# Performance work log

Hardware: AMD Instinct MI355X
Metric: run time of the kernel (lower is better)

## Reference

```python
import jax, jax.numpy as jnp
import numpy as np

B, S, E, O, LAYERS = 256, 28, 256, 256, 3


def setup_inputs() -> dict:
    key = jax.random.key(0)
    ks = jax.random.split(key, 20)
    sc = 0.05
    inp = {
        "centers": jax.random.normal(ks[0], (B, S, 3), jnp.float32),
        "object_embedding": jax.random.normal(ks[1], (B, S, E), jnp.float32),
        "counts": jax.random.randint(ks[2], (B,), 1, S + 1),
        # linear_relation_object: 3 -> E
        "Wr": jax.random.normal(ks[3], (E, 3), jnp.float32) * sc,
        "br": jnp.zeros((E,), jnp.float32),
        # LSTM (PyTorch gate order i,f,g,o)
        "W_ih": jax.random.normal(ks[4], (4 * O, E), jnp.float32) * sc,
        "W_hh": jax.random.normal(ks[5], (4 * O, O), jnp.float32) * sc,
        "b_ih": jnp.zeros((4 * O,), jnp.float32),
        "b_hh": jnp.zeros((4 * O,), jnp.float32),
        # gr: 3E -> O
        "Wgr": jax.random.normal(ks[6], (O, 3 * E), jnp.float32) * sc,
        "bgr": jnp.zeros((O,), jnp.float32),
        # bezier control: O -> O, plus scalar alpha
        "Wbc": jax.random.normal(ks[7], (O, O), jnp.float32) * sc,
        "bbc": jnp.zeros((O,), jnp.float32),
        "alpha": jnp.asarray(0.5, jnp.float32),
        # esa: E -> O
        "Wesa": jax.random.normal(ks[8], (O, E), jnp.float32) * sc,
        "besa": jnp.zeros((O,), jnp.float32),
        # gaussian heads: O -> 3
        "Wmu": jax.random.normal(ks[9], (3, O), jnp.float32) * sc,
        "bmu": jnp.zeros((3,), jnp.float32),
        "Wlv": jax.random.normal(ks[10], (3, O), jnp.float32) * sc,
        "blv": jnp.zeros((3,), jnp.float32),
    }
    return inp


def _lstm(x, W_ih, W_hh, b_ih, b_hh):
    # x: [B,S,E] -> hs: [B,S,O], zero initial state, PyTorch gate order i,f,g,o
    Bdim = x.shape[0]
    Odim = W_hh.shape[1]
    b = b_ih + b_hh

    def step(carry, xt):
        h, c = carry
        z = xt @ W_ih.T + h @ W_hh.T + b  # [B,4O]
        i, f, g, o = jnp.split(z, 4, axis=-1)
        c = jax.nn.sigmoid(f) * c + jax.nn.sigmoid(i) * jnp.tanh(g)
        h = jax.nn.sigmoid(o) * jnp.tanh(c)
        return (h, c), h

    h0 = jnp.zeros((Bdim, Odim), x.dtype)
    _, hs = jax.lax.scan(step, (h0, h0), jnp.swapaxes(x, 0, 1))
    return jnp.swapaxes(hs, 0, 1)


def reference(centers, object_embedding, counts, Wr, br, W_ih, W_hh, b_ih, b_hh,
              Wgr, bgr, Wbc, bbc, alpha, Wesa, besa, Wmu, bmu, Wlv, blv):
    # masks from per-scene object counts (padding replication of the torch loops)
    idx = jnp.arange(S)
    obj_mask = (idx[None, :] < counts[:, None]).astype(jnp.float32)[..., None]  # [B,S,1]
    rel_mask = (obj_mask[:, :, None, :] * obj_mask[:, None, :, :])              # [B,S,S,1]

    centers_p = centers * obj_mask                     # padded centers are zero
    relation = centers_p[:, :, None, :] - centers_p[:, None, :, :]  # [B,S,S,3]
    rlf = relation @ Wr.T + br                         # [B,S,S,E]

    olf = object_embedding * obj_mask                  # [B,S,E]
    t = jax.nn.sigmoid(alpha)

    for _ in range(LAYERS):
        new_olf = _lstm(olf, W_ih, W_hh, b_ih, b_hh) * obj_mask
        rep_i = jnp.broadcast_to(olf[:, :, None, :], (olf.shape[0], S, S, olf.shape[-1]))
        rep_j = jnp.broadcast_to(olf[:, None, :, :], (olf.shape[0], S, S, olf.shape[-1]))
        cat = jnp.concatenate([rep_i, rep_j, rlf], axis=-1)   # [B,S,S,3E]
        rlf_lin = cat @ Wgr.T + bgr                           # [B,S,S,O]
        cp = rlf_lin @ Wbc.T + bbc
        bez = ((1 - t) ** 2 + t ** 2) * rlf_lin + 2 * (1 - t) * t * cp
        rlf = jnp.tanh(bez) * rel_mask
        olf = new_olf

    rlf = rlf @ Wesa.T + besa                                  # [B,S,S,O]
    # base attention: softmax over dim=1 (explicit max-subtract as in source)
    base_attn = jax.nn.softmax(rlf - jnp.max(rlf, axis=1, keepdims=True), axis=1)
    # gaussian attention (eval mode: eps = 0 -> samples = mus)
    mus = rlf @ Wmu.T + bmu                                    # [B,S,S,3]
    _logvars = rlf @ Wlv.T + blv                               # computed, unused at eval
    gscores = jnp.mean(mus, axis=-1, keepdims=True)            # [B,S,S,1]
    gattn = jax.nn.softmax(gscores, axis=1)
    attn = 0.5 * base_attn + 0.5 * gattn                       # broadcast over O
    rel_out = jnp.sum(attn * rlf, axis=-2) * obj_mask          # [B,S,O]
    return rel_out
```

## Files before the change

kernel.cpp:

```cpp
#include <hip/hip_runtime.h>


typedef __attribute__((ext_vector_type(8))) short short8;
typedef __attribute__((ext_vector_type(4))) float f32x4;

__device__ __forceinline__ float b2f(unsigned short u){
  union { unsigned int i; float f; } v; v.i = ((unsigned int)u) << 16; return v.f;
}
__device__ __forceinline__ float u2f(unsigned int u){
  union { unsigned int i; float f; } v; v.i = u; return v.f;
}
__device__ __forceinline__ unsigned short f2b(float f){
  union { float f; unsigned int i; } v; v.f = f;
  return (unsigned short)((v.i + 0x8000u) >> 16);
}
__device__ __forceinline__ unsigned int pk2(float lo, float hi){
  union { float f; unsigned int i; } a, b; a.f = lo; b.f = hi;
  return __builtin_amdgcn_perm(b.i + 0x8000u, a.i + 0x8000u, 0x07060302u);
}
__device__ __forceinline__ float sigm(float x){ return 1.f/(1.f+__expf(-x)); }
__device__ __forceinline__ float tanh_f(float x){ float e = __expf(2.f*x); return 1.f - 2.f/(e+1.f); }
__device__ __forceinline__ int xsw(int row, int n){
  int c = n >> 3;
  int pc = (c & 24) | ((c ^ row) & 7);
  return row*256 + pc*8 + (n & 7);
}

#define MFMA16(a,b,c) __builtin_amdgcn_mfma_f32_16x16x32_bf16((a),(b),(c),0,0,0)

__global__ __launch_bounds__(256) void k_repack7(const float* __restrict__ Wih,
                                                 const float* __restrict__ Whh,
                                                 const float* __restrict__ Wgr,
                                                 const float* __restrict__ Wbc,
                                                 const float* __restrict__ Wesa,
                                                 const float* __restrict__ Wmu,
                                                 unsigned short* __restrict__ wcv,
                                                 float* __restrict__ wmean){
  int i = blockIdx.x*256 + threadIdx.x;
  if (i >= 851968){
    int o = i - 851968;
    if (o < 256) wmean[o] = (Wmu[o] + Wmu[256+o] + Wmu[512+o]) * (1.f/3.f);
    return;
  }
  const float* s; int segbase, N, stride, off, local;
  if      (i < 262144){ s=Wih;  segbase=0;      N=1024; stride=256; off=0;   local=i; }
  else if (i < 524288){ s=Whh;  segbase=262144; N=1024; stride=256; off=0;   local=i-262144; }
  else if (i < 589824){ s=Wgr;  segbase=524288; N=256;  stride=768; off=0;   local=i-524288; }
  else if (i < 655360){ s=Wgr;  segbase=589824; N=256;  stride=768; off=256; local=i-589824; }
  else if (i < 720896){ s=Wgr;  segbase=655360; N=256;  stride=768; off=512; local=i-655360; }
  else if (i < 786432){ s=Wbc;  segbase=720896; N=256;  stride=256; off=0;   local=i-720896; }
  else                { s=Wesa; segbase=786432; N=256;  stride=256; off=0;   local=i-786432; }
  int n = local >> 8, k = local & 255;
  wcv[segbase + (((k >> 3)*N + n) << 3) + (k & 7)] = f2b(s[n*stride + off + k]);
}

__global__ __launch_bounds__(256) void k_prep(const float* __restrict__ emb,
                                              const int* __restrict__ counts,
                                              unsigned short* __restrict__ olf,
                                              float* __restrict__ out){
  int bs = blockIdx.x;
  int b = bs / 28; int s = bs - b*28;
  int e = threadIdx.x;
  olf[(size_t)bs*256 + e] = (s < counts[b]) ? f2b(emb[(size_t)bs*256 + e]) : (unsigned short)0;
  out[(size_t)bs*256 + e] = 0.f;
}

__global__ __launch_bounds__(256) void k_xgemm(const unsigned short* __restrict__ olf,
                                               const unsigned short* __restrict__ Wih,
                                               unsigned short* __restrict__ zx){
  const int tid = threadIdx.x;
  const int wid = tid >> 6, lane = tid & 63, col = lane & 15, quad = lane >> 4;
  const int m0 = (blockIdx.x >> 1)*64 + wid*16;
  const int nt0 = (blockIdx.x & 1)*32;
  short8 af[8];
  #pragma unroll
  for (int kt=0; kt<8; ++kt)
    af[kt] = *(const short8*)&olf[(size_t)(m0 + col)*256 + kt*32 + quad*8];
  #pragma unroll 4
  for (int nt=nt0; nt<nt0+32; ++nt){
    int n = nt*16 + col;
    f32x4 acc = (f32x4){0.f,0.f,0.f,0.f};
    #pragma unroll
    for (int kt=0; kt<8; ++kt){
      short8 bf = *(const short8*)&Wih[((((kt*4 + quad) << 10) + n) << 3)];
      acc = MFMA16(bf, af[kt], acc);
    }
    *(uint2*)&zx[(size_t)(m0 + col)*1024 + nt*16 + quad*4] =
        make_uint2(pk2(acc[0],acc[1]), pk2(acc[2],acc[3]));
  }
}

__global__ __launch_bounds__(1024) void k_recat(const unsigned short* __restrict__ zx,
                                                const unsigned short* __restrict__ Whh,
                                                const float* __restrict__ bih,
                                                const float* __restrict__ bhh,
                                                const int* __restrict__ counts,
                                                unsigned short* __restrict__ olf_out,
                                                const unsigned short* __restrict__ olf_at,
                                                const unsigned short* __restrict__ Wgri,
                                                const unsigned short* __restrict__ Wgrj,
                                                const float* __restrict__ bgr,
                                                unsigned short* __restrict__ At_out){
  __shared__ unsigned short Ab[2][16*264];
  const int tid = threadIdx.x;
  const int wv = tid >> 6, lane = tid & 63, col = lane & 15, quad = lane >> 4;

  if (blockIdx.x >= 16){
    const int m0 = (blockIdx.x - 16)*256 + wv*16;
    short8 af[8];
    #pragma unroll
    for (int kt=0; kt<8; ++kt)
      af[kt] = *(const short8*)&olf_at[(size_t)(m0 + col)*256 + kt*32 + quad*8];
    #pragma unroll 4
    for (int nt=0; nt<32; ++nt){
      const unsigned short* wb = (nt < 16) ? Wgri : Wgrj;
      int nb = (nt < 16) ? 0 : 256;
      int nn = (nt & 15)*16 + col;
      f32x4 bg4 = (nt < 16) ? *(const f32x4*)&bgr[(nt & 15)*16 + quad*4]
                            : (f32x4){0.f,0.f,0.f,0.f};
      f32x4 acc = (f32x4){0.f,0.f,0.f,0.f};
      #pragma unroll
      for (int kt=0; kt<8; ++kt){
        short8 bf = *(const short8*)&wb[((((kt*4 + quad) << 8) + nn) << 3)];
        acc = MFMA16(bf, af[kt], acc);
      }
      acc += bg4;
      *(uint2*)&At_out[(size_t)(m0 + col)*512 + nb + (nt & 15)*16 + quad*4] =
          make_uint2(pk2(acc[0],acc[1]), pk2(acc[2],acc[3]));
    }
    return;
  }
  const int sc0 = blockIdx.x * 16;
  const int u = wv*16 + col;
  float bz[4];
  #pragma unroll
  for (int g=0; g<4; ++g) bz[g] = bih[g*256+u] + bhh[g*256+u];
  int cnt4[4];
  #pragma unroll
  for (int r=0; r<4; ++r) cnt4[r] = counts[sc0 + quad*4 + r];

  float cst[4];
  #pragma unroll
  for (int r=0; r<4; ++r) cst[r] = 0.f;
  for (int i=tid; i<16*264; i+=1024) Ab[0][i] = 0;
  __syncthreads();

  for (int t=0; t<28; ++t){
    const int cur = t & 1, nxt = cur ^ 1;
    float zxv[4][4];
    #pragma unroll
    for (int g=0; g<4; ++g){
      #pragma unroll
      for (int r=0; r<4; ++r)
        zxv[g][r] = b2f(zx[((size_t)(sc0 + quad*4 + r)*28 + t)*1024 + g*256 + u]);
    }
    f32x4 acc[4];
    #pragma unroll
    for (int g=0; g<4; ++g) acc[g] = (f32x4){0.f,0.f,0.f,0.f};
    #pragma unroll
    for (int kt=0; kt<8; ++kt){
      short8 a = *(const short8*)&Ab[cur][col*264 + kt*32 + quad*8];
      #pragma unroll
      for (int g=0; g<4; ++g){
        short8 bf = *(const short8*)&Whh[((((kt*4 + quad) << 10) + g*256 + u) << 3)];
        acc[g] = MFMA16(a, bf, acc[g]);
      }
    }
    #pragma unroll
    for (int r=0; r<4; ++r){
      int s = quad*4 + r;
      float zi = acc[0][r] + zxv[0][r] + bz[0];
      float zf = acc[1][r] + zxv[1][r] + bz[1];
      float zg = acc[2][r] + zxv[2][r] + bz[2];
      float zo = acc[3][r] + zxv[3][r] + bz[3];
      float cc = sigm(zf)*cst[r] + sigm(zi)*tanh_f(zg);
      cst[r] = cc;
      float hh = sigm(zo)*tanh_f(cc);
      unsigned short hb = f2b(hh);
      Ab[nxt][s*264 + u] = hb;
      olf_out[((size_t)(sc0+s)*28 + t)*256 + u] = (t < cnt4[r]) ? hb : (unsigned short)0;
    }
    __syncthreads();
  }
}

__global__ __launch_bounds__(256) void k_aterm(const unsigned short* __restrict__ olf,
                                               const unsigned short* __restrict__ Wgri,
                                               const unsigned short* __restrict__ Wgrj,
                                               const float* __restrict__ bgr,
                                               unsigned short* __restrict__ Aout){
  const int tid = threadIdx.x;
  const int wid = tid >> 6, lane = tid & 63, col = lane & 15, quad = lane >> 4;
  const int m0 = blockIdx.x*64 + wid*16;
  short8 af[8];
  #pragma unroll
  for (int kt=0; kt<8; ++kt)
    af[kt] = *(const short8*)&olf[(size_t)(m0 + col)*256 + kt*32 + quad*8];
  #pragma unroll 4
  for (int nt=0; nt<32; ++nt){
    const unsigned short* wb = (nt < 16) ? Wgri : Wgrj;
    int nb = (nt < 16) ? 0 : 256;
    int nn = (nt & 15)*16 + col;
    f32x4 bg4 = (nt < 16) ? *(const f32x4*)&bgr[(nt & 15)*16 + quad*4]
                          : (f32x4){0.f,0.f,0.f,0.f};
    f32x4 acc = (f32x4){0.f,0.f,0.f,0.f};
    #pragma unroll
    for (int kt=0; kt<8; ++kt){
      short8 bf = *(const short8*)&wb[((((kt*4 + quad) << 8) + nn) << 3)];
      acc = MFMA16(bf, af[kt], acc);
    }
    acc += bg4;
    *(uint2*)&Aout[(size_t)(m0 + col)*512 + nb + (nt & 15)*16 + quad*4] =
        make_uint2(pk2(acc[0],acc[1]), pk2(acc[2],acc[3]));
  }
}

#define GEMM_TILE64(SRC, WPTR)                                                      \
  {                                                                                 \
    _Pragma("unroll")                                                               \
    for (int rf=0; rf<4; ++rf){ Ya[rf][0]=(f32x4){0.f,0.f,0.f,0.f};                 \
                                Ya[rf][1]=(f32x4){0.f,0.f,0.f,0.f}; }               \
    _Pragma("unroll 1")                                                             \
    for (int kc=0; kc<4; ++kc){                                                     \
      short8 av[2][4], bv[2][2];                                                    \
      _Pragma("unroll")                                                             \
      for (int u=0; u<2; ++u){                                                      \
        int kt = kc*2 + u;                                                          \
        _Pragma("unroll")                                                           \
        for (int rf=0; rf<4; ++rf)                                                  \
          av[u][rf] = *(const short8*)&(SRC)[(Abase[rf] + kc*64) ^ (u*32)];         \
        bv[u][0] = *(const short8*)&(WPTR)[Bbase + kt*8192];                        \
        bv[u][1] = *(const short8*)&(WPTR)[Bbase + kt*8192 + 128];                  \
      }                                                                             \
      __builtin_amdgcn_s_setprio(1);                                                \
      _Pragma("unroll")                                                             \
      for (int u=0; u<2; ++u){                                                      \
        _Pragma("unroll")                                                           \
        for (int rf=0; rf<4; ++rf){                                                 \
          Ya[rf][0] = MFMA16(bv[u][0], av[u][rf], Ya[rf][0]);                       \
          Ya[rf][1] = MFMA16(bv[u][1], av[u][rf], Ya[rf][1]);                       \
        }                                                                           \
      }                                                                             \
      __builtin_amdgcn_s_setprio(0);                                                \
    }                                                                               \
  }

__global__ __launch_bounds__(512, 4) void k_mega(
    const float* __restrict__ centers, const int* __restrict__ counts,
    const float* __restrict__ Wr, const float* __restrict__ br,
    const unsigned short* __restrict__ Wgrr, const float* __restrict__ bgr,
    const unsigned short* __restrict__ Wbc, const float* __restrict__ bbc,
    const float* __restrict__ alpha,
    const unsigned short* __restrict__ Wesa, const float* __restrict__ besa,
    const float* __restrict__ wmean, const float* __restrict__ bmu,
    const unsigned short* __restrict__ Aterm, float* __restrict__ out){
  __shared__ unsigned short Xa[64*256];
  __shared__ unsigned short Yb[64*256];
  float* hrSBp = (float*)&Xa[56*256];
  float* gsbp  = (float*)&Xa[60*256];
  float* hrSGp = (float*)&Xa[60*256+128];
  const int tid = threadIdx.x;
  const int wv = tid >> 6;
  const int lane = tid & 63, col = lane & 15, quad = lane >> 4;
  const int xcd = blockIdx.x & 7, idx = blockIdx.x >> 3;
  const int b = xcd*32 + idx/14, jt = idx - (idx/14)*14;
  const int cb = counts[b];
  const int nbase = wv*32;

  float av_ = alpha[0];
  float tv = sigm(av_);
  float c1 = (1.f-tv)*(1.f-tv) + tv*tv;
  float c2 = 2.f*tv*(1.f-tv);

  float pv[4];
  const unsigned short* apI[4];
  const unsigned short* apJ[4];
  #pragma unroll
  for (int mt=0; mt<4; ++mt){
    int m = mt*16 + col;
    int i = m >> 1;
    int pi = (i < 27) ? i : 27;
    int pj = jt*2 + (m & 1);
    pv[mt] = (m < 56 && i < cb && pj < cb) ? 1.f : 0.f;
    apI[mt] = Aterm + (size_t)(b*28 + pi)*512 + nbase + quad*4;
    apJ[mt] = Aterm + (size_t)(b*28 + pj)*512 + 256 + nbase + quad*4;
  }
  int Abase[4];
  #pragma unroll
  for (int rf=0; rf<4; ++rf){
    int row = rf*16 + col;
    Abase[rf] = row*256 + ((quad ^ (row & 3)) | (row & 4))*8;
  }
  const int Bbase = (quad*256 + nbase + col)*8;
  int woff[4][2];
  f32x4 cbb[2], bev[2];
  #pragma unroll
  for (int nt2=0; nt2<2; ++nt2){
    int n0 = nbase + nt2*16 + quad*4;
    cbb[nt2] = (*(const f32x4*)&bbc[n0]) * c2;
    bev[nt2] = *(const f32x4*)&besa[n0];
    #pragma unroll
    for (int mt=0; mt<4; ++mt)
      woff[mt][nt2] = xsw(mt*16 + col, n0);
  }

  {
    int m = tid >> 3, sub = tid & 7;
    int i = m >> 1, j = jt*2 + (m & 1);
    bool valid = (m < 56);
    float mi = (valid && i < cb) ? 1.f : 0.f;
    float mj = (valid && j < cb) ? 1.f : 0.f;
    float vm = valid ? 1.f : 0.f;
    const float* ci = centers + (b*28 + (valid ? i : 0))*3;
    const float* cj = centers + (b*28 + j)*3;
    float dx = mi*ci[0] - mj*cj[0];
    float dy = mi*ci[1] - mj*cj[1];
    float dz = mi*ci[2] - mj*cj[2];
    #pragma unroll
    for (int c8=0; c8<4; ++c8){
      int e0 = sub*32 + c8*8;
      f32x4 w0 = *(const f32x4*)&Wr[e0*3 +  0];
      f32x4 w1 = *(const f32x4*)&Wr[e0*3 +  4];
      f32x4 w2 = *(const f32x4*)&Wr[e0*3 +  8];
      f32x4 w3 = *(const f32x4*)&Wr[e0*3 + 12];
      f32x4 w4 = *(const f32x4*)&Wr[e0*3 + 16];
      f32x4 w5 = *(const f32x4*)&Wr[e0*3 + 20];
      f32x4 b0 = *(const f32x4*)&br[e0];
      f32x4 b1 = *(const f32x4*)&br[e0+4];
      b0 *= vm; b1 *= vm;
      float v0 = dx*w0[0] + dy*w0[1] + dz*w0[2] + b0[0];
      float v1 = dx*w0[3] + dy*w1[0] + dz*w1[1] + b0[1];
      float v2 = dx*w1[2] + dy*w1[3] + dz*w2[0] + b0[2];
      float v3 = dx*w2[1] + dy*w2[2] + dz*w2[3] + b0[3];
      float v4 = dx*w3[0] + dy*w3[1] + dz*w3[2] + b1[0];
      float v5 = dx*w3[3] + dy*w4[0] + dz*w4[1] + b1[1];
      float v6 = dx*w4[2] + dy*w4[3] + dz*w5[0] + b1[2];
      float v7 = dx*w5[1] + dy*w5[2] + dz*w5[3] + b1[3];
      uint4 pw;
      pw.x = pk2(v0,v1); pw.y = pk2(v2,v3); pw.z = pk2(v4,v5); pw.w = pk2(v6,v7);
      *(uint4*)&Xa[xsw(m, e0)] = pw;
    }
  }
  __syncthreads();

  f32x4 Ya[4][2];
  #pragma unroll 1
  for (int l=0; l<3; ++l){
    uint2 rAi[4][2], rAj[4][2];
    #pragma unroll
    for (int mt=0; mt<4; ++mt){
      rAi[mt][0] = *(const uint2*)&apI[mt][0];
      rAi[mt][1] = *(const uint2*)&apI[mt][16];
      rAj[mt][0] = *(const uint2*)&apJ[mt][0];
      rAj[mt][1] = *(const uint2*)&apJ[mt][16];
      apI[mt] += 7168*512; apJ[mt] += 7168*512;
    }
    GEMM_TILE64(Xa, Wgrr);
    #pragma unroll
    for (int nt2=0; nt2<2; ++nt2){
      #pragma unroll
      for (int mt=0; mt<4; ++mt){
        uint2 wi = rAi[mt][nt2], wj = rAj[mt][nt2];
        f32x4 ai, aj;
        ai[0] = u2f(wi.x << 16); ai[1] = u2f(wi.x & 0xffff0000u);
        ai[2] = u2f(wi.y << 16); ai[3] = u2f(wi.y & 0xffff0000u);
        aj[0] = u2f(wj.x << 16); aj[1] = u2f(wj.x & 0xffff0000u);
        aj[2] = u2f(wj.y << 16); aj[3] = u2f(wj.y & 0xffff0000u);
        f32x4 v = Ya[mt][nt2] + ai + aj;
        *(uint2*)&Yb[woff[mt][nt2]] = make_uint2(pk2(v[0],v[1]), pk2(v[2],v[3]));
      }
    }
    __syncthreads();
    GEMM_TILE64(Yb, Wbc);
    #pragma unroll
    for (int nt2=0; nt2<2; ++nt2){
      #pragma unroll
      for (int mt=0; mt<4; ++mt){
        uint2 w = *(const uint2*)&Yb[woff[mt][nt2]];
        f32x4 rl;
        rl[0] = u2f(w.x << 16); rl[1] = u2f(w.x & 0xffff0000u);
        rl[2] = u2f(w.y << 16); rl[3] = u2f(w.y & 0xffff0000u);
        f32x4 bez = Ya[mt][nt2]*c2 + cbb[nt2];
        bez = rl*c1 + bez;
        float x0 = tanh_f(bez[0]) * pv[mt];
        float x1 = tanh_f(bez[1]) * pv[mt];
        float x2 = tanh_f(bez[2]) * pv[mt];
        float x3 = tanh_f(bez[3]) * pv[mt];
        *(uint2*)&Xa[woff[mt][nt2]] = make_uint2(pk2(x0,x1), pk2(x2,x3));
      }
    }
    __syncthreads();
  }
  GEMM_TILE64(Xa, Wesa);
  __syncthreads();
  f32x4 sbp[2] = {(f32x4){0.f,0.f,0.f,0.f}, (f32x4){0.f,0.f,0.f,0.f}};
  const float m3f = (col < 8) ? 1.f : 0.f;
  #pragma unroll
  for (int nt2=0; nt2<2; ++nt2){
    #pragma unroll
    for (int mt=0; mt<4; ++mt){
      f32x4 v = Ya[mt][nt2] + bev[nt2];
      *(uint2*)&Yb[woff[mt][nt2]] = make_uint2(pk2(v[0],v[1]), pk2(v[2],v[3]));
      f32x4 e;
      e[0] = __expf(v[0]); e[1] = __expf(v[1]);
      e[2] = __expf(v[2]); e[3] = __expf(v[3]);
      *(uint2*)&Xa[woff[mt][nt2]] = make_uint2(pk2(e[0],e[1]), pk2(e[2],e[3]));
      f32x4 wsum = e;
      if (mt == 3) wsum *= m3f;
      sbp[nt2] += wsum;
    }
  }
  f32x4 hr[2];
  #pragma unroll
  for (int nt2=0; nt2<2; ++nt2){
    #pragma unroll
    for (int r=0; r<4; ++r){
      float s = sbp[nt2][r];
      s += __shfl_xor(s, 2, 64);
      s += __shfl_xor(s, 4, 64);
      s += __shfl_xor(s, 8, 64);
      hr[nt2][r] = 0.5f / s;
    }
  }
  __syncthreads();
  {
    int m = tid >> 3, sub = tid & 7;
    if (m < 56){
      float s = 0.f;
      #pragma unroll
      for (int c8=0; c8<4; ++c8){
        int e0 = sub*32 + c8*8;
        uint4 u = *(const uint4*)&Yb[xsw(m, e0)];
        f32x4 wm0 = *(const f32x4*)&wmean[e0];
        f32x4 wm1 = *(const f32x4*)&wmean[e0+4];
        s += u2f(u.x << 16)*wm0[0] + u2f(u.x & 0xffff0000u)*wm0[1]
           + u2f(u.y << 16)*wm0[2] + u2f(u.y & 0xffff0000u)*wm0[3]
           + u2f(u.z << 16)*wm1[0] + u2f(u.z & 0xffff0000u)*wm1[1]
           + u2f(u.w << 16)*wm1[2] + u2f(u.w & 0xffff0000u)*wm1[3];
      }
      s += __shfl_xor(s, 1, 64);
      s += __shfl_xor(s, 2, 64);
      s += __shfl_xor(s, 4, 64);
      if (sub == 0)
        gsbp[m] = __expf(s + (bmu[0] + bmu[1] + bmu[2])*(1.f/3.f));
    }
  }
  if (col < 2){
    #pragma unroll
    for (int nt2=0; nt2<2; ++nt2){
      #pragma unroll
      for (int r=0; r<4; ++r)
        hrSBp[col*256 + nbase + nt2*16 + quad*4 + r] = hr[nt2][r];
    }
  }
  __syncthreads();
  if (tid < 2){
    int jc = tid;
    float se = 0.f;
    for (int i=0;i<28;++i) se += gsbp[i*2+jc];
    hrSGp[jc] = 0.5f / se;
  }
  __syncthreads();
  for (int it = tid; it < 7168; it += 512){
    int i = it >> 8, o = it & 255;
    if (i < cb){
      float s = 0.f;
      #pragma unroll
      for (int jc=0; jc<2; ++jc){
        int row = i*2 + jc;
        int off = xsw(row, o);
        float v = b2f(Yb[off]);
        float E = b2f(Xa[off]);
        float a = E*hrSBp[jc*256+o] + gsbp[row]*hrSGp[jc];
        s += a * v;
      }
      atomicAdd(&out[((size_t)b*28 + i)*256 + o], s);
    }
  }
}

extern "C" void kernel_launch(void* const* d_in, const int* in_sizes, int n_in,
                              void* d_out, int out_size, void* d_ws, size_t ws_size,
                              hipStream_t stream){
  const float* centers = (const float*)d_in[0];
  const float* emb     = (const float*)d_in[1];
  const int*   counts  = (const int*)d_in[2];
  const float* Wr      = (const float*)d_in[3];
  const float* br      = (const float*)d_in[4];
  const float* Wih     = (const float*)d_in[5];
  const float* Whh     = (const float*)d_in[6];
  const float* bih     = (const float*)d_in[7];
  const float* bhh     = (const float*)d_in[8];
  const float* Wgr     = (const float*)d_in[9];
  const float* bgr     = (const float*)d_in[10];
  const float* Wbc     = (const float*)d_in[11];
  const float* bbc     = (const float*)d_in[12];
  const float* alpha   = (const float*)d_in[13];
  const float* Wesa    = (const float*)d_in[14];
  const float* besa    = (const float*)d_in[15];
  const float* Wmu     = (const float*)d_in[16];
  const float* bmu     = (const float*)d_in[17];

  unsigned short* olf   = (unsigned short*)d_ws;
  unsigned short* At    = (unsigned short*)((char*)d_ws + 11010048);
  unsigned short* zx    = (unsigned short*)((char*)d_ws + 33030144);
  unsigned short* wcv   = (unsigned short*)((char*)d_ws + 47710208);
  float*          wmean = (float*)((char*)d_ws + 49414144);
  unsigned short* cWih  = wcv;
  unsigned short* cWhh  = wcv + 262144;
  unsigned short* cWgri = wcv + 524288;
  unsigned short* cWgrj = wcv + 589824;
  unsigned short* cWgrr = wcv + 655360;
  unsigned short* cWbc  = wcv + 720896;
  unsigned short* cWesa = wcv + 786432;
  float* outp = (float*)d_out;

  unsigned short* olf1 = olf + (size_t)7168*256;
  unsigned short* olf2 = olf + (size_t)2*7168*256;
  unsigned short* At1  = At  + (size_t)7168*512;
  unsigned short* At2  = At  + (size_t)2*7168*512;

  hipLaunchKernelGGL(k_repack7, dim3(3329), dim3(256), 0, stream,
                     Wih, Whh, Wgr, Wbc, Wesa, Wmu, wcv, wmean);
  hipLaunchKernelGGL(k_prep, dim3(7168), dim3(256), 0, stream, emb, counts, olf, outp);
  hipLaunchKernelGGL(k_xgemm, dim3(224), dim3(256), 0, stream, olf, cWih, zx);
  hipLaunchKernelGGL(k_recat, dim3(44), dim3(1024), 0, stream,
                     zx, cWhh, bih, bhh, counts, olf1, olf, cWgri, cWgrj, bgr, At);
  hipLaunchKernelGGL(k_xgemm, dim3(224), dim3(256), 0, stream, olf1, cWih, zx);
  hipLaunchKernelGGL(k_recat, dim3(44), dim3(1024), 0, stream,
                     zx, cWhh, bih, bhh, counts, olf2, olf1, cWgri, cWgrj, bgr, At1);
  hipLaunchKernelGGL(k_aterm, dim3(112), dim3(256), 0, stream, olf2, cWgri, cWgrj, bgr, At2);
  hipLaunchKernelGGL(k_mega,  dim3(3584), dim3(512), 0, stream,
                     centers, counts, Wr, br, cWgrr, bgr, cWbc, bbc, alpha,
                     cWesa, besa, wmean, bmu, At, outp);
}
```

Measured before the change: 1.178 ms.

## Fuse LSTM input projection into recurrent kernel and merge prep with repack

Removes the separate input-projection GEMM kernel and its zx intermediate buffer. The recurrent kernel now stages each timestep's input rows in shared memory and computes x·W_ih with MFMA alongside h·W_hh. The embedding prep kernel is folded into the weight repack launch as extra blocks. This saves launches and global traffic, but doubles the matrix work and weight reads inside the sequential 28-step loop that runs on only 16 blocks.

```diff
diff --git a/kernel.cpp b/kernel.cpp
--- a/kernel.cpp
+++ b/kernel.cpp
@@ -28,14 +28,26 @@
 
 #define MFMA16(a,b,c) __builtin_amdgcn_mfma_f32_16x16x32_bf16((a),(b),(c),0,0,0)
 
-__global__ __launch_bounds__(256) void k_repack7(const float* __restrict__ Wih,
-                                                 const float* __restrict__ Whh,
-                                                 const float* __restrict__ Wgr,
-                                                 const float* __restrict__ Wbc,
-                                                 const float* __restrict__ Wesa,
-                                                 const float* __restrict__ Wmu,
-                                                 unsigned short* __restrict__ wcv,
-                                                 float* __restrict__ wmean){
+__global__ __launch_bounds__(256) void k_reprep(const float* __restrict__ Wih,
+                                                const float* __restrict__ Whh,
+                                                const float* __restrict__ Wgr,
+                                                const float* __restrict__ Wbc,
+                                                const float* __restrict__ Wesa,
+                                                const float* __restrict__ Wmu,
+                                                unsigned short* __restrict__ wcv,
+                                                float* __restrict__ wmean,
+                                                const float* __restrict__ emb,
+                                                const int* __restrict__ counts,
+                                                unsigned short* __restrict__ olf,
+                                                float* __restrict__ out){
+  if (blockIdx.x >= 3329){
+    int bs = blockIdx.x - 3329;
+    int b = bs / 28; int s = bs - b*28;
+    int e = threadIdx.x;
+    olf[(size_t)bs*256 + e] = (s < counts[b]) ? f2b(emb[(size_t)bs*256 + e]) : (unsigned short)0;
+    out[(size_t)bs*256 + e] = 0.f;
+    return;
+  }
   int i = blockIdx.x*256 + threadIdx.x;
   if (i >= 851968){
     int o = i - 851968;
@@ -54,54 +66,19 @@
   wcv[segbase + (((k >> 3)*N + n) << 3) + (k & 7)] = f2b(s[n*stride + off + k]);
 }
 
-__global__ __launch_bounds__(256) void k_prep(const float* __restrict__ emb,
-                                              const int* __restrict__ counts,
-                                              unsigned short* __restrict__ olf,
-                                              float* __restrict__ out){
-  int bs = blockIdx.x;
-  int b = bs / 28; int s = bs - b*28;
-  int e = threadIdx.x;
-  olf[(size_t)bs*256 + e] = (s < counts[b]) ? f2b(emb[(size_t)bs*256 + e]) : (unsigned short)0;
-  out[(size_t)bs*256 + e] = 0.f;
-}
-
-__global__ __launch_bounds__(256) void k_xgemm(const unsigned short* __restrict__ olf,
-                                               const unsigned short* __restrict__ Wih,
-                                               unsigned short* __restrict__ zx){
-  const int tid = threadIdx.x;
-  const int wid = tid >> 6, lane = tid & 63, col = lane & 15, quad = lane >> 4;
-  const int m0 = (blockIdx.x >> 1)*64 + wid*16;
-  const int nt0 = (blockIdx.x & 1)*32;
-  short8 af[8];
-  #pragma unroll
-  for (int kt=0; kt<8; ++kt)
-    af[kt] = *(const short8*)&olf[(size_t)(m0 + col)*256 + kt*32 + quad*8];
-  #pragma unroll 4
-  for (int nt=nt0; nt<nt0+32; ++nt){
-    int n = nt*16 + col;
-    f32x4 acc = (f32x4){0.f,0.f,0.f,0.f};
-    #pragma unroll
-    for (int kt=0; kt<8; ++kt){
-      short8 bf = *(const short8*)&Wih[((((kt*4 + quad) << 10) + n) << 3)];
-      acc = MFMA16(bf, af[kt], acc);
-    }
-    *(uint2*)&zx[(size_t)(m0 + col)*1024 + nt*16 + quad*4] =
-        make_uint2(pk2(acc[0],acc[1]), pk2(acc[2],acc[3]));
-  }
-}
-
-__global__ __launch_bounds__(1024) void k_recat(const unsigned short* __restrict__ zx,
+__global__ __launch_bounds__(1024) void k_recat(const unsigned short* __restrict__ Wih,
                                                 const unsigned short* __restrict__ Whh,
                                                 const float* __restrict__ bih,
                                                 const float* __restrict__ bhh,
                                                 const int* __restrict__ counts,
                                                 unsigned short* __restrict__ olf_out,
-                                                const unsigned short* __restrict__ olf_at,
+                                                const unsigned short* __restrict__ olf_in,
                                                 const unsigned short* __restrict__ Wgri,
                                                 const unsigned short* __restrict__ Wgrj,
                                                 const float* __restrict__ bgr,
                                                 unsigned short* __restrict__ At_out){
   __shared__ unsigned short Ab[2][16*264];
+  __shared__ unsigned short Xb[2][16*264];
   const int tid = threadIdx.x;
   const int wv = tid >> 6, lane = tid & 63, col = lane & 15, quad = lane >> 4;
 
@@ -110,7 +87,7 @@
     short8 af[8];
     #pragma unroll
     for (int kt=0; kt<8; ++kt)
-      af[kt] = *(const short8*)&olf_at[(size_t)(m0 + col)*256 + kt*32 + quad*8];
+      af[kt] = *(const short8*)&olf_in[(size_t)(m0 + col)*256 + kt*32 + quad*8];
     #pragma unroll 4
     for (int nt=0; nt<32; ++nt){
       const unsigned short* wb = (nt < 16) ? Wgri : Wgrj;
@@ -143,36 +120,46 @@
   #pragma unroll
   for (int r=0; r<4; ++r) cst[r] = 0.f;
   for (int i=tid; i<16*264; i+=1024) Ab[0][i] = 0;
+  {
+    int row = tid >> 6, c4 = (tid & 63) << 2;
+    *(uint2*)&Xb[0][row*264 + c4] =
+        *(const uint2*)&olf_in[((size_t)(sc0 + row)*28 + 0)*256 + c4];
+  }
   __syncthreads();
 
   for (int t=0; t<28; ++t){
     const int cur = t & 1, nxt = cur ^ 1;
-    float zxv[4][4];
+    if (t < 27){
+      int row = tid >> 6, c4 = (tid & 63) << 2;
+      *(uint2*)&Xb[nxt][row*264 + c4] =
+          *(const uint2*)&olf_in[((size_t)(sc0 + row)*28 + (t+1))*256 + c4];
+    }
+    f32x4 acc[4], ac2[4];
     #pragma unroll
     for (int g=0; g<4; ++g){
-      #pragma unroll
-      for (int r=0; r<4; ++r)
-        zxv[g][r] = b2f(zx[((size_t)(sc0 + quad*4 + r)*28 + t)*1024 + g*256 + u]);
-    }
-    f32x4 acc[4];
-    #pragma unroll
-    for (int g=0; g<4; ++g) acc[g] = (f32x4){0.f,0.f,0.f,0.f};
+      acc[g] = (f32x4){0.f,0.f,0.f,0.f};
+      ac2[g] = (f32x4){0.f,0.f,0.f,0.f};
+    }
     #pragma unroll
     for (int kt=0; kt<8; ++kt){
       short8 a = *(const short8*)&Ab[cur][col*264 + kt*32 + quad*8];
+      short8 x = *(const short8*)&Xb[cur][col*264 + kt*32 + quad*8];
       #pragma unroll
       for (int g=0; g<4; ++g){
-        short8 bf = *(const short8*)&Whh[((((kt*4 + quad) << 10) + g*256 + u) << 3)];
-        acc[g] = MFMA16(a, bf, acc[g]);
+        int wix = ((((kt*4 + quad) << 10) + g*256 + u) << 3);
+        short8 bh = *(const short8*)&Whh[wix];
+        short8 bx = *(const short8*)&Wih[wix];
+        acc[g] = MFMA16(a, bh, acc[g]);
+        ac2[g] = MFMA16(x, bx, ac2[g]);
       }
     }
     #pragma unroll
     for (int r=0; r<4; ++r){
       int s = quad*4 + r;
-      float zi = acc[0][r] + zxv[0][r] + bz[0];
-      float zf = acc[1][r] + zxv[1][r] + bz[1];
-      float zg = acc[2][r] + zxv[2][r] + bz[2];
-      float zo = acc[3][r] + zxv[3][r] + bz[3];
+      float zi = acc[0][r] + ac2[0][r] + bz[0];
+      float zf = acc[1][r] + ac2[1][r] + bz[1];
+      float zg = acc[2][r] + ac2[2][r] + bz[2];
+      float zo = acc[3][r] + ac2[3][r] + bz[3];
       float cc = sigm(zf)*cst[r] + sigm(zi)*tanh_f(zg);
       cst[r] = cc;
       float hh = sigm(zo)*tanh_f(cc);
@@ -503,7 +490,6 @@
 
   unsigned short* olf   = (unsigned short*)d_ws;
   unsigned short* At    = (unsigned short*)((char*)d_ws + 11010048);
-  unsigned short* zx    = (unsigned short*)((char*)d_ws + 33030144);
   unsigned short* wcv   = (unsigned short*)((char*)d_ws + 47710208);
   float*          wmean = (float*)((char*)d_ws + 49414144);
   unsigned short* cWih  = wcv;
@@ -520,15 +506,13 @@
   unsigned short* At1  = At  + (size_t)7168*512;
   unsigned short* At2  = At  + (size_t)2*7168*512;
 
-  hipLaunchKernelGGL(k_repack7, dim3(3329), dim3(256), 0, stream,
-                     Wih, Whh, Wgr, Wbc, Wesa, Wmu, wcv, wmean);
-  hipLaunchKernelGGL(k_prep, dim3(7168), dim3(256), 0, stream, emb, counts, olf, outp);
-  hipLaunchKernelGGL(k_xgemm, dim3(224), dim3(256), 0, stream, olf, cWih, zx);
+  hipLaunchKernelGGL(k_reprep, dim3(10497), dim3(256), 0, stream,
+                     Wih, Whh, Wgr, Wbc, Wesa, Wmu, wcv, wmean,
+                     emb, counts, olf, outp);
   hipLaunchKernelGGL(k_recat, dim3(44), dim3(1024), 0, stream,
-                     zx, cWhh, bih, bhh, counts, olf1, olf, cWgri, cWgrj, bgr, At);
-  hipLaunchKernelGGL(k_xgemm, dim3(224), dim3(256), 0, stream, olf1, cWih, zx);
+                     cWih, cWhh, bih, bhh, counts, olf1, olf, cWgri, cWgrj, bgr, At);
   hipLaunchKernelGGL(k_recat, dim3(44), dim3(1024), 0, stream,
-                     zx, cWhh, bih, bhh, counts, olf2, olf1, cWgri, cWgrj, bgr, At1);
+                     cWih, cWhh, bih, bhh, counts, olf2, olf1, cWgri, cWgrj, bgr, At1);
   hipLaunchKernelGGL(k_aterm, dim3(112), dim3(256), 0, stream, olf2, cWgri, cWgrj, bgr, At2);
   hipLaunchKernelGGL(k_mega,  dim3(3584), dim3(512), 0, stream,
                      centers, counts, Wr, br, cWgrr, bgr, cWbc, bbc, alpha,
```

Result: slower. 2.053 ms (+74.2%).
